# Kernel optimization log

Hardware: AMD Instinct MI355X
Metric: run time of the kernel (lower is better)

The kernel has to match this reference:

```python
import jax, jax.numpy as jnp
import numpy as np

N_NODES = 50000
ELU_ALPHA = 0.2  # torch.nn.ELU(0.2): alpha=0.2


def _elu(v, alpha):
    return jnp.where(v > 0, v, alpha * jnp.expm1(v))


def setup_inputs() -> dict:
    key = jax.random.key(0)
    k1, k2, k3, k4, k5 = jax.random.split(key, 5)
    fin, H, F = 128, 4, 32
    E = 1600000
    return {
        "x": jax.random.normal(k1, (N_NODES, fin), dtype=jnp.float32),
        "W": jax.random.normal(k2, (fin, H * F), dtype=jnp.float32) * (1.414 / np.sqrt(fin)),
        "a_src": jax.random.normal(k3, (H, F), dtype=jnp.float32) * 0.1,
        "a_tgt": jax.random.normal(k4, (H, F), dtype=jnp.float32) * 0.1,
        "edge_index": jax.random.randint(k5, (E, 2), 0, N_NODES, dtype=jnp.int64),
    }


def reference(x, W, a_src, a_tgt, edge_index):
    # GAT layer (dropout omitted: eval mode). x: [N, fin]
    N = x.shape[0]
    H, F = a_src.shape
    xp = (x @ W).reshape(N, H, F)                 # projected node feats [N,H,F]
    s_src = jnp.einsum("nhf,hf->nh", xp, a_src)   # per-head source scores [N,H]
    s_tgt = jnp.einsum("nhf,hf->nh", xp, a_tgt)   # per-head target scores [N,H]

    src = edge_index[:, 0]
    tgt = edge_index[:, 1]

    # edge-wise gather (the memory-bound hotspot)
    e = _elu(s_src[src] + s_tgt[tgt], ELU_ALPHA)  # [E,H]

    # segment softmax over edges sharing a target node
    m = jax.ops.segment_max(e, tgt, num_segments=N)           # [N,H]
    m = jnp.where(jnp.isfinite(m), m, 0.0)
    ex = jnp.exp(e - m[tgt])                                  # [E,H]
    denom = jax.ops.segment_sum(ex, tgt, num_segments=N)      # [N,H]
    alpha = ex / denom[tgt]                                   # [E,H]

    # gather source features, weight, scatter-add into target nodes
    msg = alpha[:, :, None] * xp[src]                          # [E,H,F]
    out = jax.ops.segment_sum(msg, tgt, num_segments=N)        # [N,H,F]
    return out.reshape(N, H * F)                               # concat heads
```

## Files before the change

kernel.cpp:

```cpp
#include <hip/hip_runtime.h>
#include <hip/hip_bf16.h>
#include <math.h>

#define FIN 128
#define NHEAD 4
#define CH 128
#define ELU_A 0.2f

#define BSHIFT 8
#define NB 196
#define CAP 16384
#define T_EDGES 2048

typedef unsigned int uint32;
typedef __attribute__((ext_vector_type(8))) short short8;
typedef __attribute__((ext_vector_type(4))) float f32x4;

__device__ __forceinline__ float bf16lo(uint32 u) {
    union { uint32 i; float f; } c; c.i = u << 16; return c.f;
}
__device__ __forceinline__ float bf16hi(uint32 u) {
    union { uint32 i; float f; } c; c.i = u & 0xffff0000u; return c.f;
}
__device__ __forceinline__ unsigned short f2b(float f) {
    union { float f; uint32 u; } c; c.f = f;
    uint32 u = c.u;
    return (unsigned short)((u + 0x7fffu + ((u >> 16) & 1u)) >> 16);
}

union SMem {
    struct {
        uint32 stage[T_EDGES];
        int hist[256], scanbuf[256], loff[256], cnt2[256], base[256];
    } p;
    unsigned short wt[128][136];
    unsigned short cbuf[4][16][132];
};

__global__ __launch_bounds__(256) void mega_kernel(
    const int2* __restrict__ ei2, int* __restrict__ bcnt,
    uint32* __restrict__ ebuck, const float* __restrict__ x,
    const float* __restrict__ W, unsigned short* __restrict__ xpb,
    const float* __restrict__ a_src, const float* __restrict__ a_tgt,
    float* __restrict__ s_src, float* __restrict__ s_tgt,
    int E, int N, int PB)
{
    __shared__ SMem sm;
    const int tid = threadIdx.x;

    if ((int)blockIdx.x < PB) {
        const int e0 = blockIdx.x * T_EDGES;
        const int tile = min(T_EDGES, E - e0);

        sm.p.hist[tid] = 0; sm.p.cnt2[tid] = 0;
        __syncthreads();

        uint32 rec[8];
#pragma unroll
        for (int j = 0; j < 8; ++j) {
            int idx = e0 + j * 256 + tid;
            if (idx < E) {
                int2 p = ei2[idx];
                rec[j] = (uint32)p.x | ((uint32)p.y << 16);
                atomicAdd(&sm.p.hist[p.y >> BSHIFT], 1);
            } else rec[j] = 0xFFFFFFFFu;
        }
        __syncthreads();

        sm.p.scanbuf[tid] = sm.p.hist[tid];
        __syncthreads();
        for (int off = 1; off < 256; off <<= 1) {
            int v = (tid >= off) ? sm.p.scanbuf[tid - off] : 0;
            __syncthreads();
            sm.p.scanbuf[tid] += v;
            __syncthreads();
        }
        sm.p.loff[tid] = sm.p.scanbuf[tid] - sm.p.hist[tid];
        if (tid < NB && sm.p.hist[tid] > 0)
            sm.p.base[tid] = tid * CAP + atomicAdd(&bcnt[tid], sm.p.hist[tid]);
        __syncthreads();

#pragma unroll
        for (int j = 0; j < 8; ++j) {
            if (rec[j] != 0xFFFFFFFFu) {
                int b = rec[j] >> (16 + BSHIFT);
                int r = atomicAdd(&sm.p.cnt2[b], 1);
                sm.p.stage[sm.p.loff[b] + r] = rec[j];
            }
        }
        __syncthreads();

        for (int i = tid; i < tile; i += 256) {
            uint32 rc = sm.p.stage[i];
            int b = rc >> (16 + BSHIFT);
            ebuck[(size_t)sm.p.base[b] + (i - sm.p.loff[b])] = rc;
        }
        return;
    }

    const int gb = blockIdx.x - PB;

    for (int i = tid; i < FIN * CH / 2; i += 256) {
        int n  = i & 127;
        int k2 = i >> 7;
        float w0 = W[(size_t)(2 * k2 + 0) * CH + n];
        float w1 = W[(size_t)(2 * k2 + 1) * CH + n];
        uint32 pk = (uint32)f2b(w0) | ((uint32)f2b(w1) << 16);
        *(uint32*)&sm.wt[n][2 * k2] = pk;
    }
    __syncthreads();

    const int lane = tid & 63;
    const int wid  = tid >> 6;
    const int rowbase = gb * 64 + wid * 16;

    const int rr   = min(rowbase + (lane & 15), N - 1);
    const int krow = (lane >> 4) * 8;

    f32x4 acc[8];
#pragma unroll
    for (int c = 0; c < 8; ++c) acc[c] = (f32x4){0.f, 0.f, 0.f, 0.f};

#pragma unroll
    for (int s = 0; s < 4; ++s) {
        const int koff = s * 32 + krow;
        const float* xr = x + (size_t)rr * FIN + koff;
        float4 p0 = *(const float4*)xr;
        float4 p1 = *(const float4*)(xr + 4);
        short8 af;
        af[0] = (short)f2b(p0.x); af[1] = (short)f2b(p0.y);
        af[2] = (short)f2b(p0.z); af[3] = (short)f2b(p0.w);
        af[4] = (short)f2b(p1.x); af[5] = (short)f2b(p1.y);
        af[6] = (short)f2b(p1.z); af[7] = (short)f2b(p1.w);
#pragma unroll
        for (int c = 0; c < 8; ++c) {
            const short8 bf = *(const short8*)&sm.wt[c * 16 + (lane & 15)][koff];
            acc[c] = __builtin_amdgcn_mfma_f32_16x16x32_bf16(af, bf, acc[c], 0, 0, 0);
        }
    }
    __syncthreads();

#pragma unroll
    for (int c = 0; c < 8; ++c)
#pragma unroll
        for (int r = 0; r < 4; ++r)
            sm.cbuf[wid][(lane >> 4) * 4 + r][c * 16 + (lane & 15)] = f2b(acc[c][r]);
    __syncthreads();

    for (int r = 0; r < 16; ++r) {
        int row = rowbase + r;
        if (row < N) {
            uint32 v = *(const uint32*)&sm.cbuf[wid][r][lane * 2];
            *(uint32*)&xpb[(size_t)row * CH + lane * 2] = v;
        }
    }

    {
        const int srow = lane >> 2;
        const int sh   = lane & 3;
        const unsigned short* cp = &sm.cbuf[wid][srow][sh * 32];
        const float* as = a_src + sh * 32;
        const float* at = a_tgt + sh * 32;
        float ps = 0.f, pt = 0.f;
#pragma unroll
        for (int q = 0; q < 4; ++q) {
            uint4 u = *(const uint4*)&cp[q * 8];
            float4 a0 = *(const float4*)&as[q * 8];
            float4 a1 = *(const float4*)&as[q * 8 + 4];
            float4 b0 = *(const float4*)&at[q * 8];
            float4 b1 = *(const float4*)&at[q * 8 + 4];
            float l0 = bf16lo(u.x), h0 = bf16hi(u.x);
            float l1 = bf16lo(u.y), h1 = bf16hi(u.y);
            float l2 = bf16lo(u.z), h2 = bf16hi(u.z);
            float l3 = bf16lo(u.w), h3 = bf16hi(u.w);
            ps += l0*a0.x + h0*a0.y + l1*a0.z + h1*a0.w
                + l2*a1.x + h2*a1.y + l3*a1.z + h3*a1.w;
            pt += l0*b0.x + h0*b0.y + l1*b0.z + h1*b0.w
                + l2*b1.x + h2*b1.y + l3*b1.z + h3*b1.w;
        }
        int node = rowbase + srow;
        if (node < N) {
            s_src[(size_t)node * NHEAD + sh] = ps;
            s_tgt[(size_t)node * NHEAD + sh] = pt;
        }
    }
}

__global__ __launch_bounds__(1024) void fine_scatter_kernel(
    const uint32* __restrict__ ebuck, const int* __restrict__ bcnt,
    int* __restrict__ deg, int* __restrict__ rowptr,
    int* __restrict__ srcs, int N)
{
    __shared__ int ldeg[256], psum[256], lcur[256], red[256];
    const int B    = blockIdx.x >> 1;
    const int half = blockIdx.x & 1;
    const int tid  = threadIdx.x;

    if (tid < 256) {
        red[tid]  = (tid < B) ? bcnt[tid] : 0;
        ldeg[tid] = 0;
    }
    __syncthreads();
    for (int off = 128; off >= 1; off >>= 1) {
        if (tid < off) red[tid] += red[tid + off];
        __syncthreads();
    }
    const int gb = red[0];

    const int cnt = bcnt[B];
    const uint32* rp = ebuck + (size_t)B * CAP;

    for (int i = tid; i < cnt; i += 1024)
        atomicAdd(&ldeg[(rp[i] >> 16) & 255], 1);
    __syncthreads();

    if (tid < 256) psum[tid] = ldeg[tid];
    __syncthreads();
    for (int off = 1; off < 256; off <<= 1) {
        int u = 0;
        if (tid < 256 && tid >= off) u = psum[tid - off];
        __syncthreads();
        if (tid < 256) psum[tid] += u;
        __syncthreads();
    }

    if (tid < 256) {
        int pref = gb + psum[tid] - ldeg[tid];
        lcur[tid] = pref;
        int node = B * 256 + tid;
        if ((tid >> 7) == half && node < N) {
            deg[node] = ldeg[tid];
            rowptr[node] = pref;
        }
    }
    __syncthreads();

    for (int i = tid; i < cnt; i += 1024) {
        uint32 rc = rp[i];
        int local = (rc >> 16) & 255;
        if ((local >> 7) == half) {
            int pos = atomicAdd(&lcur[local], 1);
            srcs[pos] = rc & 0xffff;
        }
    }
}

__global__ __launch_bounds__(256) void aggregate_kernel(
    const int* __restrict__ srcs, const int* __restrict__ rowptr,
    const int* __restrict__ deg, const float* __restrict__ s_src,
    const float* __restrict__ s_tgt, const uint32* __restrict__ xpb,
    float* __restrict__ out, int N)
{
    const int lane = threadIdx.x & 63;
    const int wid  = __builtin_amdgcn_readfirstlane(threadIdx.x >> 6);
    const int t = blockIdx.x * 4 + wid;
    if (t >= N) return;

    const int start = __builtin_amdgcn_readfirstlane(rowptr[t]);
    const int d     = __builtin_amdgcn_readfirstlane(deg[t]);
    const int h     = lane >> 4;
    const float st_h = s_tgt[(size_t)t * NHEAD + h];

    float accx = 0.0f, accy = 0.0f, dsum = 0.0f;
    int k = 0;

#define ACC(E, X) { dsum += (E); accx += (E) * bf16lo(X); accy += (E) * bf16hi(X); }

    const int cj16 = lane & 15;
    const int bb16 = h * 16;
    for (; k + 16 <= d; k += 16) {
        int   sv = srcs[start + k + cj16];
        float a  = s_src[(size_t)sv * NHEAD + h];
        float v  = a + st_h;
        float u  = v > 0.0f ? v : ELU_A * (__expf(v) - 1.0f);
        float e  = __expf(u);

        int s0 = srcs[start + k + 0],  s1 = srcs[start + k + 1];
        int s2 = srcs[start + k + 2],  s3 = srcs[start + k + 3];
        int s4 = srcs[start + k + 4],  s5 = srcs[start + k + 5];
        int s6 = srcs[start + k + 6],  s7 = srcs[start + k + 7];
        int s8 = srcs[start + k + 8],  s9 = srcs[start + k + 9];
        int sa = srcs[start + k + 10], sb = srcs[start + k + 11];
        int sc = srcs[start + k + 12], sd = srcs[start + k + 13];
        int se = srcs[start + k + 14], sf = srcs[start + k + 15];

        uint32 x0 = xpb[(size_t)s0 * 64 + lane], x1 = xpb[(size_t)s1 * 64 + lane];
        uint32 x2 = xpb[(size_t)s2 * 64 + lane], x3 = xpb[(size_t)s3 * 64 + lane];
        uint32 x4 = xpb[(size_t)s4 * 64 + lane], x5 = xpb[(size_t)s5 * 64 + lane];
        uint32 x6 = xpb[(size_t)s6 * 64 + lane], x7 = xpb[(size_t)s7 * 64 + lane];
        uint32 x8 = xpb[(size_t)s8 * 64 + lane], x9 = xpb[(size_t)s9 * 64 + lane];
        uint32 xa = xpb[(size_t)sa * 64 + lane], xb = xpb[(size_t)sb * 64 + lane];
        uint32 xc = xpb[(size_t)sc * 64 + lane], xd = xpb[(size_t)sd * 64 + lane];
        uint32 xe = xpb[(size_t)se * 64 + lane], xf = xpb[(size_t)sf * 64 + lane];

        float e0 = __shfl(e, bb16 + 0),  e1 = __shfl(e, bb16 + 1);
        float e2 = __shfl(e, bb16 + 2),  e3 = __shfl(e, bb16 + 3);
        float e4 = __shfl(e, bb16 + 4),  e5 = __shfl(e, bb16 + 5);
        float e6 = __shfl(e, bb16 + 6),  e7 = __shfl(e, bb16 + 7);
        float e8 = __shfl(e, bb16 + 8),  e9 = __shfl(e, bb16 + 9);
        float ea = __shfl(e, bb16 + 10), eb = __shfl(e, bb16 + 11);
        float ec = __shfl(e, bb16 + 12), ed = __shfl(e, bb16 + 13);
        float ee = __shfl(e, bb16 + 14), ef = __shfl(e, bb16 + 15);

        ACC(e0, x0) ACC(e1, x1) ACC(e2, x2) ACC(e3, x3)
        ACC(e4, x4) ACC(e5, x5) ACC(e6, x6) ACC(e7, x7)
        ACC(e8, x8) ACC(e9, x9) ACC(ea, xa) ACC(eb, xb)
        ACC(ec, xc) ACC(ed, xd) ACC(ee, xe) ACC(ef, xf)
    }

    const int cj8 = lane & 7;
    const int chh = (lane >> 3) & 3;
    const float st_c = s_tgt[(size_t)t * NHEAD + chh];
    const int bb8 = h * 8;
    for (; k + 8 <= d; k += 8) {
        int   sv = srcs[start + k + cj8];
        float a  = s_src[(size_t)sv * NHEAD + chh];
        float v  = a + st_c;
        float u  = v > 0.0f ? v : ELU_A * (__expf(v) - 1.0f);
        float e  = __expf(u);

        int s0 = srcs[start + k + 0], s1 = srcs[start + k + 1];
        int s2 = srcs[start + k + 2], s3 = srcs[start + k + 3];
        int s4 = srcs[start + k + 4], s5 = srcs[start + k + 5];
        int s6 = srcs[start + k + 6], s7 = srcs[start + k + 7];

        uint32 x0 = xpb[(size_t)s0 * 64 + lane], x1 = xpb[(size_t)s1 * 64 + lane];
        uint32 x2 = xpb[(size_t)s2 * 64 + lane], x3 = xpb[(size_t)s3 * 64 + lane];
        uint32 x4 = xpb[(size_t)s4 * 64 + lane], x5 = xpb[(size_t)s5 * 64 + lane];
        uint32 x6 = xpb[(size_t)s6 * 64 + lane], x7 = xpb[(size_t)s7 * 64 + lane];

        float e0 = __shfl(e, bb8 + 0), e1 = __shfl(e, bb8 + 1);
        float e2 = __shfl(e, bb8 + 2), e3 = __shfl(e, bb8 + 3);
        float e4 = __shfl(e, bb8 + 4), e5 = __shfl(e, bb8 + 5);
        float e6 = __shfl(e, bb8 + 6), e7 = __shfl(e, bb8 + 7);

        ACC(e0, x0) ACC(e1, x1) ACC(e2, x2) ACC(e3, x3)
        ACC(e4, x4) ACC(e5, x5) ACC(e6, x6) ACC(e7, x7)
    }

    for (; k < d; ++k) {
        int   s  = srcs[start + k];
        float a  = s_src[(size_t)s * NHEAD + h];
        uint32 xv = xpb[(size_t)s * 64 + lane];
        float v = a + st_h;
        float u = v > 0.0f ? v : ELU_A * (__expf(v) - 1.0f);
        float e = __expf(u);
        ACC(e, xv)
    }
#undef ACC

    float inv = (d > 0) ? 1.0f / dsum : 0.0f;
    float2 o = make_float2(accx * inv, accy * inv);
    *(float2*)&out[(size_t)t * CH + lane * 2] = o;
}

extern "C" void kernel_launch(void* const* d_in, const int* in_sizes, int n_in,
                              void* d_out, int out_size, void* d_ws, size_t ws_size,
                              hipStream_t stream)
{
    const float* x     = (const float*)d_in[0];
    const float* W     = (const float*)d_in[1];
    const float* a_src = (const float*)d_in[2];
    const float* a_tgt = (const float*)d_in[3];
    const int*   ei    = (const int*)d_in[4];

    const int N = in_sizes[0] / FIN;
    const int E = in_sizes[4] / 2;
    const int PB = (E + T_EDGES - 1) / T_EDGES;
    const int GB = (N + 63) / 64;

    char* ws = (char*)d_ws;
    unsigned short* xpb = (unsigned short*)ws;  ws += (size_t)N * CH * sizeof(unsigned short);
    float* s_src  = (float*)ws;                 ws += (size_t)N * NHEAD * sizeof(float);
    float* s_tgt  = (float*)ws;                 ws += (size_t)N * NHEAD * sizeof(float);
    int*   deg    = (int*)ws;                   ws += (size_t)N * sizeof(int);
    int*   bcnt   = (int*)ws;                   ws += (size_t)NB * sizeof(int);
    int*   rowptr = (int*)ws;                   ws += (size_t)N * sizeof(int);
    int*   srcs   = (int*)ws;                   ws += (size_t)E * sizeof(int);
    uint32* ebuck = (uint32*)ws;                ws += (size_t)NB * CAP * sizeof(uint32);

    float* out = (float*)d_out;
    const int2* ei2 = (const int2*)ei;

    hipMemsetAsync(bcnt, 0, (size_t)NB * sizeof(int), stream);

    mega_kernel<<<PB + GB, 256, 0, stream>>>(
        ei2, bcnt, ebuck, x, W, xpb, a_src, a_tgt, s_src, s_tgt, E, N, PB);
    fine_scatter_kernel<<<NB * 2, 1024, 0, stream>>>(
        ebuck, bcnt, deg, rowptr, srcs, N);
    aggregate_kernel<<<(N + 3) / 4, 256, 0, stream>>>(
        srcs, rowptr, deg, s_src, s_tgt, (const uint32*)xpb, out, N);
}
```

Measured before the change: 121.1 us.

## Use wave-shuffle scan, vectorized W loads, and packed rowptr/degree metadata

```diff
diff --git a/kernel.cpp b/kernel.cpp
--- a/kernel.cpp
+++ b/kernel.cpp
@@ -27,11 +27,14 @@
     uint32 u = c.u;
     return (unsigned short)((u + 0x7fffu + ((u >> 16) & 1u)) >> 16);
 }
+__device__ __forceinline__ uint32 pack2(float a, float b) {
+    return (uint32)f2b(a) | ((uint32)f2b(b) << 16);
+}
 
 union SMem {
     struct {
         uint32 stage[T_EDGES];
-        int hist[256], scanbuf[256], loff[256], cnt2[256], base[256];
+        int hist[256], loff[256], cnt2[256], base[256], wsum[4];
     } p;
     unsigned short wt[128][136];
     unsigned short cbuf[4][16][132];
@@ -67,17 +70,25 @@
         }
         __syncthreads();
 
-        sm.p.scanbuf[tid] = sm.p.hist[tid];
-        __syncthreads();
-        for (int off = 1; off < 256; off <<= 1) {
-            int v = (tid >= off) ? sm.p.scanbuf[tid - off] : 0;
+        {
+            int v = sm.p.hist[tid];
+            int scan = v;
+            const int lane = tid & 63;
+#pragma unroll
+            for (int off = 1; off < 64; off <<= 1) {
+                int tmp = __shfl_up(scan, off);
+                if (lane >= off) scan += tmp;
+            }
+            if (lane == 63) sm.p.wsum[tid >> 6] = scan;
             __syncthreads();
-            sm.p.scanbuf[tid] += v;
-            __syncthreads();
-        }
-        sm.p.loff[tid] = sm.p.scanbuf[tid] - sm.p.hist[tid];
-        if (tid < NB && sm.p.hist[tid] > 0)
-            sm.p.base[tid] = tid * CAP + atomicAdd(&bcnt[tid], sm.p.hist[tid]);
+            int base = 0;
+#pragma unroll
+            for (int w = 0; w < 4; ++w)
+                base += (w < (tid >> 6)) ? sm.p.wsum[w] : 0;
+            sm.p.loff[tid] = scan + base - v;
+            if (tid < NB && v > 0)
+                sm.p.base[tid] = tid * CAP + atomicAdd(&bcnt[tid], v);
+        }
         __syncthreads();
 
 #pragma unroll
@@ -100,13 +111,15 @@
 
     const int gb = blockIdx.x - PB;
 
-    for (int i = tid; i < FIN * CH / 2; i += 256) {
-        int n  = i & 127;
-        int k2 = i >> 7;
-        float w0 = W[(size_t)(2 * k2 + 0) * CH + n];
-        float w1 = W[(size_t)(2 * k2 + 1) * CH + n];
-        uint32 pk = (uint32)f2b(w0) | ((uint32)f2b(w1) << 16);
-        *(uint32*)&sm.wt[n][2 * k2] = pk;
+    for (int task = tid; task < 64 * 32; task += 256) {
+        int k2 = task >> 5;
+        int n4 = (task & 31) * 4;
+        float4 w0 = *(const float4*)&W[(size_t)(2 * k2 + 0) * CH + n4];
+        float4 w1 = *(const float4*)&W[(size_t)(2 * k2 + 1) * CH + n4];
+        *(uint32*)&sm.wt[n4 + 0][2 * k2] = pack2(w0.x, w1.x);
+        *(uint32*)&sm.wt[n4 + 1][2 * k2] = pack2(w0.y, w1.y);
+        *(uint32*)&sm.wt[n4 + 2][2 * k2] = pack2(w0.z, w1.z);
+        *(uint32*)&sm.wt[n4 + 3][2 * k2] = pack2(w0.w, w1.w);
     }
     __syncthreads();
 
@@ -188,8 +201,7 @@
 
 __global__ __launch_bounds__(1024) void fine_scatter_kernel(
     const uint32* __restrict__ ebuck, const int* __restrict__ bcnt,
-    int* __restrict__ deg, int* __restrict__ rowptr,
-    int* __restrict__ srcs, int N)
+    int2* __restrict__ meta, int* __restrict__ srcs, int N)
 {
     __shared__ int ldeg[256], psum[256], lcur[256], red[256];
     const int B    = blockIdx.x >> 1;
@@ -228,10 +240,8 @@
         int pref = gb + psum[tid] - ldeg[tid];
         lcur[tid] = pref;
         int node = B * 256 + tid;
-        if ((tid >> 7) == half && node < N) {
-            deg[node] = ldeg[tid];
-            rowptr[node] = pref;
-        }
+        if ((tid >> 7) == half && node < N)
+            meta[node] = make_int2(pref, ldeg[tid]);
     }
     __syncthreads();
 
@@ -246,18 +256,18 @@
 }
 
 __global__ __launch_bounds__(256) void aggregate_kernel(
-    const int* __restrict__ srcs, const int* __restrict__ rowptr,
-    const int* __restrict__ deg, const float* __restrict__ s_src,
-    const float* __restrict__ s_tgt, const uint32* __restrict__ xpb,
-    float* __restrict__ out, int N)
+    const int* __restrict__ srcs, const int2* __restrict__ meta,
+    const float* __restrict__ s_src, const float* __restrict__ s_tgt,
+    const uint32* __restrict__ xpb, float* __restrict__ out, int N)
 {
     const int lane = threadIdx.x & 63;
     const int wid  = __builtin_amdgcn_readfirstlane(threadIdx.x >> 6);
     const int t = blockIdx.x * 4 + wid;
     if (t >= N) return;
 
-    const int start = __builtin_amdgcn_readfirstlane(rowptr[t]);
-    const int d     = __builtin_amdgcn_readfirstlane(deg[t]);
+    const int2 m    = meta[t];
+    const int start = __builtin_amdgcn_readfirstlane(m.x);
+    const int d     = __builtin_amdgcn_readfirstlane(m.y);
     const int h     = lane >> 4;
     const float st_h = s_tgt[(size_t)t * NHEAD + h];
 
@@ -373,9 +383,8 @@
     unsigned short* xpb = (unsigned short*)ws;  ws += (size_t)N * CH * sizeof(unsigned short);
     float* s_src  = (float*)ws;                 ws += (size_t)N * NHEAD * sizeof(float);
     float* s_tgt  = (float*)ws;                 ws += (size_t)N * NHEAD * sizeof(float);
-    int*   deg    = (int*)ws;                   ws += (size_t)N * sizeof(int);
+    int2*  meta   = (int2*)ws;                  ws += (size_t)N * sizeof(int2);
     int*   bcnt   = (int*)ws;                   ws += (size_t)NB * sizeof(int);
-    int*   rowptr = (int*)ws;                   ws += (size_t)N * sizeof(int);
     int*   srcs   = (int*)ws;                   ws += (size_t)E * sizeof(int);
     uint32* ebuck = (uint32*)ws;                ws += (size_t)NB * CAP * sizeof(uint32);
 
@@ -387,7 +396,7 @@
     mega_kernel<<<PB + GB, 256, 0, stream>>>(
         ei2, bcnt, ebuck, x, W, xpb, a_src, a_tgt, s_src, s_tgt, E, N, PB);
     fine_scatter_kernel<<<NB * 2, 1024, 0, stream>>>(
-        ebuck, bcnt, deg, rowptr, srcs, N);
+        ebuck, bcnt, meta, srcs, N);
     aggregate_kernel<<<(N + 3) / 4, 256, 0, stream>>>(
-        srcs, rowptr, deg, s_src, s_tgt, (const uint32*)xpb, out, N);
-}
+        srcs, meta, s_src, s_tgt, (const uint32*)xpb, out, N);
+}
```

Result: no change. 122.7 us (+1.3%).
